# Performance work log

Hardware: AMD Instinct MI355X
Metric: run time of the kernel (lower is better)

## Reference

```python
import jax, jax.numpy as jnp
import numpy as np

N = 1024          # grid resolution (grid.shape = (N, N))
B = 8             # batch size
VISCOSITY = 1e-3
DRAG = 0.1
DT = 1e-3         # time step passed to forward(vort_hat, dt)

# Carpenter-Kennedy low-storage RK4 / Crank-Nicolson coefficients
ALPHAS = (0.0, 0.1496590219993, 0.3704009573644, 0.6222557631345, 0.9582821306748, 1.0)
BETAS = (0.0, -0.4178904745, -1.192151694643, -1.697784692471, -1.514183444257)
GAMMAS = (0.1496590219993, 0.3792103129999, 0.8229550293869, 0.6994504559488, 0.1530572479681)


def _rfft_mesh(n):
    # integer wavenumbers on unit domain: fftfreq along x, rfftfreq along y (last axis)
    kx1 = jnp.fft.fftfreq(n, d=1.0 / n).astype(jnp.float32)
    ky1 = jnp.fft.rfftfreq(n, d=1.0 / n).astype(jnp.float32)
    kx, ky = jnp.meshgrid(kx1, ky1, indexing='ij')  # (n, n//2+1)
    return kx, ky


def _brick_wall_filter(n):
    # 2/3-rule dealiasing filter, exactly as in brick_wall_filter_2d
    filt = np.zeros((n, n // 2 + 1), dtype=np.float32)
    a = int(2 / 3 * n) // 2
    b = int(2 / 3 * (n // 2 + 1))
    filt[:a, :b] = 1.0
    filt[-a:, :b] = 1.0
    return jnp.asarray(filt)


def setup_inputs() -> dict:
    key = jax.random.key(0)
    w0 = jax.random.normal(key, (B, N, N), dtype=jnp.float32)
    return {"w0": w0}


def reference(w0):
    kx, ky = _rfft_mesh(N)                       # (N, N//2+1) each
    k2 = kx * kx + ky * ky
    laplace = -(2.0 * jnp.pi) ** 2 * k2          # (2*pi*i)^2 * k^2, real-valued
    linear_term = VISCOSITY * laplace - DRAG     # implicit (diffusion + drag) multiplier
    lap_safe = laplace.at[0, 0].set(1.0)         # avoid div-by-zero for mean mode
    filt = _brick_wall_filter(N)
    two_pi_i = 2j * jnp.pi

    def explicit_terms(wh):
        # vorticity -> velocity via stream function
        psi_hat = -wh / lap_safe
        vx = jnp.fft.irfft2(two_pi_i * ky * psi_hat, s=(N, N))
        vy = jnp.fft.irfft2(-two_pi_i * kx * psi_hat, s=(N, N))
        # spectral gradient of vorticity
        gx = jnp.fft.irfft2(two_pi_i * kx * wh, s=(N, N))
        gy = jnp.fft.irfft2(two_pi_i * ky * wh, s=(N, N))
        advection = -(gx * vx + gy * vy)
        return jnp.fft.rfft2(advection) * filt   # smooth=True: 2/3-rule dealiasing

    vort_hat = jnp.fft.rfft2(w0)                 # (B, N, N//2+1) complex64

    # low-storage RK4 / Crank-Nicolson stepping
    u = vort_hat
    h = jnp.zeros_like(u)
    for k in range(len(BETAS)):
        h = explicit_terms(u) + BETAS[k] * h
        mu = 0.5 * DT * (ALPHAS[k + 1] - ALPHAS[k])
        u = (u + GAMMAS[k] * DT * h + mu * linear_term * u) / (1.0 - mu * linear_term)

    dvortdt_hat = (u - vort_hat) / DT
    # pack complex outputs (vort_hat_new, dvortdt_hat) into one real array
    return jnp.stack([u.real, u.imag, dvortdt_hat.real, dvortdt_hat.imag], axis=0)
```

## Files before the change

### kernel.cpp

```cpp
#include <hip/hip_runtime.h>
#include <math.h>

static constexpr int N  = 1024;
static constexpr int NH = 513;
static constexpr int P  = 520;
static constexpr int B  = 8;
static constexpr size_t PPLANE = (size_t)B * N * P;
static constexpr size_t LPLANE = (size_t)B * N * NH;
static constexpr int SLOT = 1089;

__device__ __forceinline__ float2 cmul(float2 a, float2 b){
  return make_float2(a.x*b.x - a.y*b.y, a.x*b.y + a.y*b.x);
}
__device__ __forceinline__ int sw(int e){ return e + (e >> 4); }

template<int DIR, int GT>
__device__ void fftq(float2* s, const float2* __restrict__ tw, int lane){
  for (int i = lane; i < 1024; i += GT){
    int j = (int)(__brev((unsigned)i) >> 22);
    if (j > i){ float2 t = s[sw(i)]; s[sw(i)] = s[sw(j)]; s[sw(j)] = t; }
  }
  __syncthreads();
  #pragma unroll
  for (int st = 0; st < 10; st += 2){
    const int h = 1 << st;
    for (int q = lane; q < 256; q += GT){
      int j  = q & (h - 1);
      int g  = ((q >> st) << (st + 2)) | j;
      int i0 = sw(g), i1 = sw(g + h), i2 = sw(g + 2*h), i3 = sw(g + 3*h);
      float2 A = s[i0], Bv = s[i1], C = s[i2], D = s[i3];
      float2 w1 = tw[j << (9 - st)];
      float2 w2 = tw[j << (8 - st)];
      if (DIR < 0){ w1.y = -w1.y; w2.y = -w2.y; }
      float2 t1 = cmul(w1, Bv);
      float2 A1 = make_float2(A.x + t1.x, A.y + t1.y);
      float2 B1 = make_float2(A.x - t1.x, A.y - t1.y);
      float2 t2 = cmul(w1, D);
      float2 C1 = make_float2(C.x + t2.x, C.y + t2.y);
      float2 D1 = make_float2(C.x - t2.x, C.y - t2.y);
      float2 t3 = cmul(w2, C1);
      float2 t4c = cmul(w2, D1);
      float2 t4 = (DIR > 0) ? make_float2(t4c.y, -t4c.x) : make_float2(-t4c.y, t4c.x);
      s[i0] = make_float2(A1.x + t3.x, A1.y + t3.y);
      s[i2] = make_float2(A1.x - t3.x, A1.y - t3.y);
      s[i1] = make_float2(B1.x + t4.x, B1.y + t4.y);
      s[i3] = make_float2(B1.x - t4.x, B1.y - t4.y);
    }
    __syncthreads();
  }
}

__global__ __launch_bounds__(256) void init_tw(float2* tw){
  int i = blockIdx.x * 256 + threadIdx.x;
  if (i < 512){
    double ang = -2.0 * M_PI * (double)i / 1024.0;
    tw[i] = make_float2((float)cos(ang), (float)sin(ang));
  }
}

__global__ __launch_bounds__(256) void row_r2c_pack(const float* __restrict__ in,
                                                    float2* __restrict__ out,
                                                    const float2* __restrict__ tw){
  __shared__ float2 s[1088];
  const int tid = threadIdx.x;
  size_t pr = blockIdx.x;
  const float* p0 = in + pr * 2048;
  const float* p1 = p0 + 1024;
  for (int i = tid; i < 1024; i += 256) s[sw(i)] = make_float2(p0[i], p1[i]);
  __syncthreads();
  fftq<1, 256>(s, tw, tid);
  float2* q0 = out + (size_t)(2 * pr) * P;
  float2* q1 = q0 + P;
  for (int k = tid; k < NH; k += 256){
    float2 Zk = s[sw(k)];
    float2 Zm = s[sw((1024 - k) & 1023)];
    q0[k] = make_float2(0.5f * (Zk.x + Zm.x), 0.5f * (Zk.y - Zm.y));
    q1[k] = make_float2(0.5f * (Zk.y + Zm.y), 0.5f * (Zm.x - Zk.x));
  }
}

__global__ __launch_bounds__(512, 4) void col_fwd(const float2* __restrict__ in,
                                                  float2* __restrict__ out,
                                                  float2* __restrict__ out2,
                                                  const float2* __restrict__ tw){
  __shared__ float2 s[8 * SLOT];
  const int tid = threadIdx.x;
  int blk = blockIdx.x;
  int b = blk / 65, cb = (blk % 65) * 8;
  int c_l = tid & 7, r0 = tid >> 3;
  float2* sc = s + c_l * SLOT;
  const float2* p = in + (size_t)b * N * P + (cb + c_l);
  #pragma unroll
  for (int k = 0; k < 16; ++k){ int i = r0 + 64 * k; sc[sw(i)] = p[(size_t)i * P]; }
  __syncthreads();
  int g = tid >> 6, lane = tid & 63;
  fftq<1, 64>(s + g * SLOT, tw, lane);
  if (cb + c_l < NH){
    size_t base = (size_t)b * N * P + (cb + c_l);
    #pragma unroll
    for (int k = 0; k < 16; ++k){
      int i = r0 + 64 * k;
      float2 v = sc[sw(i)];
      out [base + (size_t)i * P] = v;
      out2[base + (size_t)i * P] = v;
    }
  }
}

__global__ __launch_bounds__(512, 4) void spec_col_inv(const float2* __restrict__ u,
                                                       float2* __restrict__ T0,
                                                       float2* __restrict__ T1,
                                                       float2* __restrict__ T2,
                                                       float2* __restrict__ T3,
                                                       const float2* __restrict__ tw){
  __shared__ float2 s[8 * SLOT];
  const int tid = threadIdx.x;
  int blk = blockIdx.x;
  int f = blockIdx.y;
  int b = blk / 65, cb = (blk % 65) * 8;
  int c_l = tid & 7, r0 = tid >> 3;
  int c = cb + c_l;
  int cg = min(c, 512);
  float2* sc = s + c_l * SLOT;
  const float2* p = u + (size_t)b * N * P + cg;
  const float kyc = (float)cg;
  const bool zerocol = (c == 0);
  const float TWO_PI = 6.2831853071795864769f;
  const float FOUR_PI2 = 39.478417604357434f;
  #pragma unroll
  for (int k = 0; k < 16; ++k){
    int i = r0 + 64 * k;
    float kxf = (i < 512) ? (float)i : (float)(i - 1024);
    float lap = -FOUR_PI2 * (kxf * kxf + kyc * kyc);
    float lap_safe = (i == 0 && zerocol) ? 1.f : lap;
    float m;
    if      (f == 0) m = -TWO_PI * kyc / lap_safe;
    else if (f == 1) m =  TWO_PI * kxf / lap_safe;
    else if (f == 2) m =  TWO_PI * kxf;
    else             m =  TWO_PI * kyc;
    float2 uv = p[(size_t)i * P];
    sc[sw(i)] = make_float2(-m * uv.y, m * uv.x);
  }
  __syncthreads();
  int g = tid >> 6, lane = tid & 63;
  fftq<-1, 64>(s + g * SLOT, tw, lane);
  float2* q = (f == 0) ? T0 : (f == 1) ? T1 : (f == 2) ? T2 : T3;
  if (c < NH){
    size_t base = (size_t)b * N * P + c;
    #pragma unroll
    for (int k = 0; k < 16; ++k){
      int i = r0 + 64 * k;
      q[base + (size_t)i * P] = sc[sw(i)];
    }
  }
}

__global__ __launch_bounds__(256) void row_adv_fft(const float2* __restrict__ T0,
                                                   const float2* __restrict__ T1,
                                                   const float2* __restrict__ T2,
                                                   const float2* __restrict__ T3,
                                                   float2* __restrict__ W1,
                                                   const float2* __restrict__ tw){
  __shared__ float2 s[1088];
  __shared__ float prod[1024];
  __shared__ float advr[2][1024];
  const int tid = threadIdx.x;
  int blk = blockIdx.x;
  int b = blk >> 9, qr = blk & 511;
  const float inv_n4 = 9.094947017729282e-13f;
  for (int r = 0; r < 2; ++r){
    size_t row_off = ((size_t)b * N + 2 * qr + r) * P;
    for (int pair = 0; pair < 2; ++pair){
      const float2* pa = (pair == 0 ? T0 : T1) + row_off;
      const float2* pb = (pair == 0 ? T2 : T3) + row_off;
      for (int i = tid; i < 1024; i += 256){
        float2 A, Bv;
        if (i <= 512){
          A = pa[i]; Bv = pb[i];
          if (i == 0 || i == 512){ A.y = 0.f; Bv.y = 0.f; }
          s[sw(i)] = make_float2(A.x - Bv.y, A.y + Bv.x);
        } else {
          int m = 1024 - i; A = pa[m]; Bv = pb[m];
          s[sw(i)] = make_float2(A.x + Bv.y, Bv.x - A.y);
        }
      }
      __syncthreads();
      fftq<-1, 256>(s, tw, tid);
      if (pair == 0){
        for (int i = tid; i < 1024; i += 256) prod[i] = s[sw(i)].x * s[sw(i)].y;
      } else {
        for (int i = tid; i < 1024; i += 256)
          advr[r][i] = -(prod[i] + s[sw(i)].x * s[sw(i)].y) * inv_n4;
      }
      __syncthreads();
    }
  }
  for (int i = tid; i < 1024; i += 256) s[sw(i)] = make_float2(advr[0][i], advr[1][i]);
  __syncthreads();
  fftq<1, 256>(s, tw, tid);
  float2* q0 = W1 + ((size_t)b * N + 2 * qr) * P;
  float2* q1 = q0 + P;
  for (int k = tid; k < NH; k += 256){
    float2 Zk = s[sw(k)];
    float2 Zm = s[sw((1024 - k) & 1023)];
    q0[k] = make_float2(0.5f * (Zk.x + Zm.x), 0.5f * (Zk.y - Zm.y));
    q1[k] = make_float2(0.5f * (Zk.y + Zm.y), 0.5f * (Zm.x - Zk.x));
  }
}

__global__ __launch_bounds__(512, 4) void col_fwd_update(const float2* __restrict__ A,
                                                         float2* __restrict__ u,
                                                         float2* __restrict__ h,
                                                         const float2* __restrict__ tw,
                                                         float gdt, float beta, float mu,
                                                         int first){
  __shared__ float2 s[8 * SLOT];
  const int tid = threadIdx.x;
  int blk = blockIdx.x;
  int b = blk / 65, cb = (blk % 65) * 8;
  int c_l = tid & 7, r0 = tid >> 3;
  float2* sc = s + c_l * SLOT;
  const float2* p = A + (size_t)b * N * P + (cb + c_l);
  #pragma unroll
  for (int k = 0; k < 16; ++k){ int i = r0 + 64 * k; sc[sw(i)] = p[(size_t)i * P]; }
  __syncthreads();
  int g = tid >> 6, lane = tid & 63;
  fftq<1, 64>(s + g * SLOT, tw, lane);
  int c = cb + c_l;
  if (c < NH){
    const bool cpass = (c < 342);
    const float kyf = (float)c;
    const float FOUR_PI2 = 39.478417604357434f;
    #pragma unroll
    for (int k = 0; k < 16; ++k){
      int x = r0 + 64 * k;
      bool pass = cpass && (x < 341 || x >= 683);
      float2 F = pass ? sc[sw(x)] : make_float2(0.f, 0.f);
      size_t off = ((size_t)b * N + x) * P + c;
      float2 hv;
      if (first) hv = F;
      else { float2 ho = h[off]; hv = make_float2(F.x + beta * ho.x, F.y + beta * ho.y); }
      h[off] = hv;
      float kxf = (x < 512) ? (float)x : (float)(x - 1024);
      float lap = -FOUR_PI2 * (kxf * kxf + kyf * kyf);
      float lin = 1e-3f * lap - 0.1f;
      float aa = 1.f + mu * lin;
      float dd = 1.f - mu * lin;
      float2 uv = u[off];
      u[off] = make_float2((uv.x * aa + gdt * hv.x) / dd,
                           (uv.y * aa + gdt * hv.y) / dd);
    }
  }
}

__global__ __launch_bounds__(256) void finalize(const float2* __restrict__ u,
                                                const float2* __restrict__ vort,
                                                float* __restrict__ out){
  size_t pi = (size_t)blockIdx.x * 256 + threadIdx.x;
  if (pi >= PPLANE) return;
  int c = (int)(pi % P);
  if (c >= NH) return;
  size_t row = pi / P;
  size_t li = row * NH + c;
  float2 uv = u[pi], vv = vort[pi];
  out[li]              = uv.x;
  out[LPLANE + li]     = uv.y;
  out[2 * LPLANE + li] = (uv.x - vv.x) * 1000.f;
  out[3 * LPLANE + li] = (uv.y - vv.y) * 1000.f;
}

extern "C" void kernel_launch(void* const* d_in, const int* in_sizes, int n_in,
                              void* d_out, int out_size, void* d_ws, size_t ws_size,
                              hipStream_t stream){
  const float* w0 = (const float*)d_in[0];
  float* out = (float*)d_out;
  char* ws = (char*)d_ws;

  const size_t CB = PPLANE * sizeof(float2);
  size_t off = 0;
  float2* tw   = (float2*)(ws + off); off += 4096;
  float2* vort = (float2*)(ws + off); off += CB;
  float2* u    = (float2*)(ws + off); off += CB;
  float2* h    = (float2*)(ws + off); off += CB;
  float2* T2   = (float2*)(ws + off); off += CB;
  float2* T3   = (float2*)(ws + off); off += CB;
  float2* W1   = (float2*)(ws + off); off += CB;
  float2* T0   = W1;
  float2* T1   = (float2*)d_out;

  const double ALPHAS[6] = {0.0, 0.1496590219993, 0.3704009573644,
                            0.6222557631345, 0.9582821306748, 1.0};
  const double BETAS[5]  = {0.0, -0.4178904745, -1.192151694643,
                            -1.697784692471, -1.514183444257};
  const double GAMMAS[5] = {0.1496590219993, 0.3792103129999, 0.8229550293869,
                            0.6994504559488, 0.1530572479681};
  const double DT = 1e-3;

  hipLaunchKernelGGL(init_tw, dim3(2), dim3(256), 0, stream, tw);

  hipLaunchKernelGGL(row_r2c_pack, dim3(B * 512), dim3(256), 0, stream, w0, W1, tw);
  hipLaunchKernelGGL(col_fwd, dim3(B * 65), dim3(512), 0, stream, W1, vort, u, tw);

  for (int k = 0; k < 5; ++k){
    float gdt  = (float)(GAMMAS[k] * DT);
    float beta = (float)BETAS[k];
    float mu   = (float)(0.5 * DT * (ALPHAS[k + 1] - ALPHAS[k]));
    hipLaunchKernelGGL(spec_col_inv, dim3(B * 65, 4), dim3(512), 0, stream,
                       u, T0, T1, T2, T3, tw);
    hipLaunchKernelGGL(row_adv_fft, dim3(B * 512), dim3(256), 0, stream,
                       T0, T1, T2, T3, W1, tw);
    hipLaunchKernelGGL(col_fwd_update, dim3(B * 65), dim3(512), 0, stream,
                       W1, u, h, tw, gdt, beta, mu, (k == 0) ? 1 : 0);
  }

  hipLaunchKernelGGL(finalize, dim3((int)((PPLANE + 255) / 256)), dim3(256), 0, stream,
                     u, vort, out);
}
```

Baseline: 1.381 ms.

## Run four row FFTs concurrently in advection kernel and interleave column-inverse block order

The advection row kernel now uses 512 threads and four shared-memory slots, running all four inverse row FFTs (two rows × two field pairs) at once instead of one after another. This removes the serialized FFT passes and their barriers. The cost is more shared memory per block, which may lower occupancy. The column-inverse launch is flattened to a 1D grid where the four fields of each group of eight panels sit next to each other, so blocks reading the same u columns run close in time and can share cache.

```diff
diff --git a/kernel.cpp b/kernel.cpp
--- a/kernel.cpp
+++ b/kernel.cpp
@@ -115,9 +115,12 @@
                                                        const float2* __restrict__ tw){
   __shared__ float2 s[8 * SLOT];
   const int tid = threadIdx.x;
-  int blk = blockIdx.x;
-  int f = blockIdx.y;
-  int b = blk / 65, cb = (blk % 65) * 8;
+  int bid = blockIdx.x;
+  int chunk = bid >> 5;
+  int idx = bid & 31;
+  int f = idx >> 3;
+  int panel = chunk * 8 + (idx & 7);
+  int b = panel / 65, cb = (panel % 65) * 8;
   int c_l = tid & 7, r0 = tid >> 3;
   int c = cb + c_l;
   int cg = min(c, 512);
@@ -155,52 +158,50 @@
   }
 }
 
-__global__ __launch_bounds__(256) void row_adv_fft(const float2* __restrict__ T0,
+__global__ __launch_bounds__(512) void row_adv_fft(const float2* __restrict__ T0,
                                                    const float2* __restrict__ T1,
                                                    const float2* __restrict__ T2,
                                                    const float2* __restrict__ T3,
                                                    float2* __restrict__ W1,
                                                    const float2* __restrict__ tw){
-  __shared__ float2 s[1088];
-  __shared__ float prod[1024];
+  __shared__ float2 s[4 * SLOT];
   __shared__ float advr[2][1024];
   const int tid = threadIdx.x;
   int blk = blockIdx.x;
   int b = blk >> 9, qr = blk & 511;
   const float inv_n4 = 9.094947017729282e-13f;
-  for (int r = 0; r < 2; ++r){
-    size_t row_off = ((size_t)b * N + 2 * qr + r) * P;
-    for (int pair = 0; pair < 2; ++pair){
-      const float2* pa = (pair == 0 ? T0 : T1) + row_off;
-      const float2* pb = (pair == 0 ? T2 : T3) + row_off;
-      for (int i = tid; i < 1024; i += 256){
-        float2 A, Bv;
-        if (i <= 512){
-          A = pa[i]; Bv = pb[i];
-          if (i == 0 || i == 512){ A.y = 0.f; Bv.y = 0.f; }
-          s[sw(i)] = make_float2(A.x - Bv.y, A.y + Bv.x);
-        } else {
-          int m = 1024 - i; A = pa[m]; Bv = pb[m];
-          s[sw(i)] = make_float2(A.x + Bv.y, Bv.x - A.y);
-        }
-      }
-      __syncthreads();
-      fftq<-1, 256>(s, tw, tid);
-      if (pair == 0){
-        for (int i = tid; i < 1024; i += 256) prod[i] = s[sw(i)].x * s[sw(i)].y;
-      } else {
-        for (int i = tid; i < 1024; i += 256)
-          advr[r][i] = -(prod[i] + s[sw(i)].x * s[sw(i)].y) * inv_n4;
-      }
-      __syncthreads();
-    }
-  }
-  for (int i = tid; i < 1024; i += 256) s[sw(i)] = make_float2(advr[0][i], advr[1][i]);
-  __syncthreads();
-  fftq<1, 256>(s, tw, tid);
+  const int u4 = tid >> 7, lane = tid & 127;
+  const int r = u4 >> 1, pair = u4 & 1;
+  size_t row_off = ((size_t)b * N + 2 * qr + r) * P;
+  const float2* pa = (pair == 0 ? T0 : T1) + row_off;
+  const float2* pb = (pair == 0 ? T2 : T3) + row_off;
+  float2* sc = s + u4 * SLOT;
+  for (int i = lane; i < 1024; i += 128){
+    float2 A, Bv;
+    if (i <= 512){
+      A = pa[i]; Bv = pb[i];
+      if (i == 0 || i == 512){ A.y = 0.f; Bv.y = 0.f; }
+      sc[sw(i)] = make_float2(A.x - Bv.y, A.y + Bv.x);
+    } else {
+      int m = 1024 - i; A = pa[m]; Bv = pb[m];
+      sc[sw(i)] = make_float2(A.x + Bv.y, Bv.x - A.y);
+    }
+  }
+  __syncthreads();
+  fftq<-1, 128>(sc, tw, lane);
+  for (int t = tid; t < 2048; t += 512){
+    int rr = t >> 10, i = t & 1023;
+    float2 a0 = s[(2 * rr) * SLOT + sw(i)];
+    float2 a1 = s[(2 * rr + 1) * SLOT + sw(i)];
+    advr[rr][i] = -(a0.x * a0.y + a1.x * a1.y) * inv_n4;
+  }
+  __syncthreads();
+  for (int i = tid; i < 1024; i += 512) s[sw(i)] = make_float2(advr[0][i], advr[1][i]);
+  __syncthreads();
+  fftq<1, 512>(s, tw, tid);
   float2* q0 = W1 + ((size_t)b * N + 2 * qr) * P;
   float2* q1 = q0 + P;
-  for (int k = tid; k < NH; k += 256){
+  for (int k = tid; k < NH; k += 512){
     float2 Zk = s[sw(k)];
     float2 Zm = s[sw((1024 - k) & 1023)];
     q0[k] = make_float2(0.5f * (Zk.x + Zm.x), 0.5f * (Zk.y - Zm.y));
@@ -305,9 +306,9 @@
     float gdt  = (float)(GAMMAS[k] * DT);
     float beta = (float)BETAS[k];
     float mu   = (float)(0.5 * DT * (ALPHAS[k + 1] - ALPHAS[k]));
-    hipLaunchKernelGGL(spec_col_inv, dim3(B * 65, 4), dim3(512), 0, stream,
+    hipLaunchKernelGGL(spec_col_inv, dim3(65 * 32), dim3(512), 0, stream,
                        u, T0, T1, T2, T3, tw);
-    hipLaunchKernelGGL(row_adv_fft, dim3(B * 512), dim3(256), 0, stream,
+    hipLaunchKernelGGL(row_adv_fft, dim3(B * 512), dim3(512), 0, stream,
                        T0, T1, T2, T3, W1, tw);
     hipLaunchKernelGGL(col_fwd_update, dim3(B * 65), dim3(512), 0, stream,
                        W1, u, h, tw, gdt, beta, mu, (k == 0) ? 1 : 0);
```

New measurement: 1.325 ms. -4.0%, faster.
